# Kernel tuning notes

Hardware: AMD Instinct MI355X
Metric: run time of the kernel (lower is better)

The kernel has to match this reference:

```python
import jax, jax.numpy as jnp
import numpy as np

N = 20000      # nodes
E = 640000     # edges
HID = 128      # hidden_dim
HEADS = 8
HD = HID // HEADS  # head_dim = 16


def setup_inputs() -> dict:
    key = jax.random.key(0)
    ks = jax.random.split(key, 32)
    s = 1.0 / np.sqrt(HID)
    d = {}
    d["h"] = jax.random.normal(ks[0], (N, HID), jnp.float32)
    d["x"] = jax.random.normal(ks[1], (N, 3), jnp.float32)
    d["src"] = jax.random.randint(ks[2], (E,), 0, N)
    d["dst"] = jax.random.randint(ks[3], (E,), 0, N)
    d["distances"] = jax.random.uniform(ks[4], (E,), jnp.float32)
    d["bpp_edge_bias"] = jax.random.uniform(ks[5], (E,), jnp.float32)
    d["msa_edge_bias"] = jax.random.uniform(ks[6], (E,), jnp.float32)
    d["chem_edge_bias"] = jax.random.uniform(ks[7], (E,), jnp.float32)
    d["relative_offset"] = jax.random.normal(ks[8], (E,), jnp.float32)
    d["chain_break_mask"] = jax.random.uniform(ks[9], (E,), jnp.float32)
    # attention projections (nn.Linear(hidden, hidden): y = x @ W + b)
    for i, nm in enumerate(["Wq", "Wk", "Wv", "Wo"]):
        d[nm] = jax.random.normal(ks[10 + i], (HID, HID), jnp.float32) * s
    for nm in ["bq", "bk", "bv", "bo"]:
        d[nm] = jnp.zeros((HID,), jnp.float32)
    # six Linear(1, heads) edge-bias heads -> weight vector [HEADS] + bias [HEADS]
    for i, nm in enumerate(["dist", "bpp", "msa", "chem", "rel", "chain"]):
        d["w_" + nm] = jax.random.normal(ks[14 + i], (HEADS,), jnp.float32) * 0.1
        d["b_" + nm] = jnp.zeros((HEADS,), jnp.float32)
    # coord_gate: Linear(HID,HID) -> SiLU -> Linear(HID,1) -> Tanh
    d["Wg1"] = jax.random.normal(ks[20], (HID, HID), jnp.float32) * s
    d["bg1"] = jnp.zeros((HID,), jnp.float32)
    d["wg2"] = jax.random.normal(ks[21], (HID, 1), jnp.float32) * s
    d["bg2"] = jnp.zeros((1,), jnp.float32)
    return d


def _edge_bias(feat, w, b):
    # Linear(1, heads) applied to per-edge scalar: [E] -> [E, HEADS]
    return feat[:, None] * w[None, :] + b[None, :]


def reference(h, x, src, dst, distances, bpp_edge_bias, msa_edge_bias,
              chem_edge_bias, relative_offset, chain_break_mask,
              Wq, bq, Wk, bk, Wv, bv, Wo, bo,
              w_dist, b_dist, w_bpp, b_bpp, w_msa, b_msa,
              w_chem, b_chem, w_rel, b_rel, w_chain, b_chain,
              Wg1, bg1, wg2, bg2):
    n = h.shape[0]
    q = (h @ Wq + bq).reshape(n, HEADS, HD)
    k = (h @ Wk + bk).reshape(n, HEADS, HD)
    v = (h @ Wv + bv).reshape(n, HEADS, HD)
    q_src = q[src]   # [E, H, D]
    k_dst = k[dst]
    v_dst = v[dst]
    logits = jnp.einsum('ehd,ehd->eh', q_src, k_dst) / np.sqrt(float(HD))
    logits = (logits
              - _edge_bias(distances * distances, w_dist, b_dist)
              + _edge_bias(bpp_edge_bias, w_bpp, b_bpp)
              + _edge_bias(msa_edge_bias, w_msa, b_msa)
              + _edge_bias(chem_edge_bias, w_chem, b_chem)
              + _edge_bias(relative_offset, w_rel, b_rel)
              + _edge_bias(chain_break_mask, w_chain, b_chain))
    # segment softmax over edges grouped by src node, per head
    m = jax.ops.segment_max(logits, src, num_segments=n)        # [N, H]
    ex = jnp.exp(logits - m[src])                               # [E, H]
    denom = jax.ops.segment_sum(ex, src, num_segments=n)        # [N, H]
    weights = ex / jnp.maximum(denom[src], 1e-9)                # [E, H]
    # weighted scatter-aggregate of values to src nodes
    h_update = jax.ops.segment_sum(v_dst * weights[:, :, None], src,
                                   num_segments=n).reshape(n, HID)
    h_out = h + h_update @ Wo + bo
    # coordinate update
    weights_mean = weights.mean(axis=1)                         # [E]
    disp = jax.ops.segment_sum((x[dst] - x[src]) * weights_mean[:, None],
                               src, num_segments=n)             # [N, 3]
    gate = jnp.tanh(jax.nn.silu(h_out @ Wg1 + bg1) @ wg2 + bg2)  # [N, 1]
    x_out = x + gate * disp
    return h_out, x_out
```

## Files before the change

### kernel.cpp

```cpp
#include <hip/hip_runtime.h>
#include <hip/hip_bf16.h>

#define N_NODES 20000
#define N_EDGES 640000
#define HID 128
#define HEADS 8
#define HD 16
#define NB_SCAN ((N_NODES + 255) / 256)
#define CH 192
#define QKV_BLOCKS 625
#define PREP_BLOCKS 2
#define NREP 32
#define HIST_OFF (PREP_BLOCKS + QKV_BLOCKS)
#define HIST_BLOCKS 128

typedef __attribute__((ext_vector_type(8))) short bf16x8;
typedef __attribute__((ext_vector_type(4))) float f32x4;

__device__ __forceinline__ float bflo(unsigned u) {
    union { unsigned i; float f; } x; x.i = u << 16; return x.f;
}
__device__ __forceinline__ float bfhi(unsigned u) {
    union { unsigned i; float f; } x; x.i = u & 0xffff0000u; return x.f;
}
__device__ __forceinline__ float bfu(ushort u) {
    union { unsigned i; float f; } x; x.i = ((unsigned)u) << 16; return x.f;
}
__device__ __forceinline__ ushort f2bu(float f) {
    __hip_bfloat16 b = __float2bfloat16(f);
    union { __hip_bfloat16 b; ushort u; } c; c.b = b; return c.u;
}

__global__ __launch_bounds__(256) void front_kernel(
        const float* __restrict__ h,
        const float* __restrict__ bq, const float* __restrict__ bk,
        const float* __restrict__ bv,
        ushort* __restrict__ qb, ushort* __restrict__ kb, ushort* __restrict__ vb,
        const int* __restrict__ src,
        int* __restrict__ cnt, int* __restrict__ rank,
        const float* __restrict__ Wq, const float* __restrict__ Wk,
        const float* __restrict__ Wv, const float* __restrict__ Wo,
        const float* __restrict__ Wg1, ushort* __restrict__ Wt) {
    __shared__ __align__(16) ushort hs[32 * 136];
    __shared__ __align__(16) ushort ws[128 * 136];
    const int t = threadIdx.x;
    if (blockIdx.x < PREP_BLOCKS) {
        const float* W = (blockIdx.x == 0) ? Wo : Wg1;
        ushort* out = Wt + (size_t)(3 + blockIdx.x) * 16384;
        for (int i = t; i < 16384; i += 256) {
            int k = i >> 7, n = i & 127;
            out[n * 128 + k] = f2bu(W[i]);
        }
    } else if (blockIdx.x < HIST_OFF) {
        const int row0 = (blockIdx.x - PREP_BLOCKS) * 32;
        for (int i = t; i < 4096; i += 256)
            hs[(i >> 7) * 136 + (i & 127)] = f2bu(h[(size_t)row0 * 128 + i]);
        __syncthreads();
        const int w = t >> 6, lane = t & 63;
        const int rt = w >> 1, half = w & 1;
        const int lrow = lane & 15, lkb = (lane >> 4) * 8;
        bf16x8 a[4];
#pragma unroll
        for (int ks = 0; ks < 4; ++ks)
            a[ks] = *reinterpret_cast<const bf16x8*>(&hs[(rt * 16 + lrow) * 136 + ks * 32 + lkb]);
        __syncthreads();
        const int rloc0 = rt * 16 + (lane >> 4) * 4;
#define DO_MAT(WSRC, BIAS, OUT) \
        { \
        for (int idx = t; idx < 8192; idx += 256) { \
            const int c = idx & 127, kp = idx >> 7; \
            const float w0 = WSRC[(2 * kp) * 128 + c]; \
            const float w1 = WSRC[(2 * kp + 1) * 128 + c]; \
            *reinterpret_cast<unsigned*>(&ws[c * 136 + 2 * kp]) = \
                (unsigned)f2bu(w0) | ((unsigned)f2bu(w1) << 16); \
        } \
        __syncthreads(); \
        for (int ctp = 0; ctp < 4; ++ctp) { \
            const int col = (ctp * 2 + half) * 16 + lrow; \
            f32x4 acc = {0.f, 0.f, 0.f, 0.f}; \
            _Pragma("unroll") \
            for (int ks = 0; ks < 4; ++ks) { \
                bf16x8 b = *reinterpret_cast<const bf16x8*>( \
                    &ws[col * 136 + ks * 32 + lkb]); \
                acc = __builtin_amdgcn_mfma_f32_16x16x32_bf16(a[ks], b, acc, 0, 0, 0); \
            } \
            const float bias = BIAS[col]; \
            _Pragma("unroll") \
            for (int r = 0; r < 4; ++r) \
                hs[(rloc0 + r) * 128 + col] = f2bu(acc[r] + bias); \
        } \
        __syncthreads(); \
        { \
            uint4* outp = reinterpret_cast<uint4*>(OUT + (size_t)row0 * 128); \
            const uint4* inp = reinterpret_cast<const uint4*>(hs); \
            outp[t] = inp[t]; \
            outp[t + 256] = inp[t + 256]; \
        } \
        __syncthreads(); \
        }
        DO_MAT(Wq, bq, qb)
        DO_MAT(Wk, bk, kb)
        DO_MAT(Wv, bv, vb)
#undef DO_MAT
    } else {
        const int b = blockIdx.x - HIST_OFF;
        for (int e = b * 256 + t; e < N_EDGES; e += HIST_BLOCKS * 256) {
            const int rep = (e >> 8) & (NREP - 1);
            rank[e] = atomicAdd(&cnt[rep * N_NODES + src[e]], 1);
        }
    }
}

__global__ __launch_bounds__(256) void scan1_kernel(const int* __restrict__ cnt,
        int* __restrict__ repOff, int* __restrict__ startp,
        int* __restrict__ blockSums, int n) {
    __shared__ int sd[256];
    const int tid = threadIdx.x;
    const int i = blockIdx.x * 256 + tid;
    int running = 0;
    if (i < n) {
#pragma unroll
        for (int r = 0; r < NREP; ++r) {
            int v = cnt[r * N_NODES + i];
            repOff[r * N_NODES + i] = running;
            running += v;
        }
    }
    sd[tid] = running;
    __syncthreads();
#pragma unroll
    for (int off = 1; off < 256; off <<= 1) {
        int tv = (tid >= off) ? sd[tid - off] : 0;
        __syncthreads();
        sd[tid] += tv;
        __syncthreads();
    }
    if (i < n) startp[i] = sd[tid] - running;
    if (tid == 255) blockSums[blockIdx.x] = sd[255];
}

__global__ __launch_bounds__(128) void scan2_kernel(int* __restrict__ blockSums, int nb) {
    __shared__ int sd[128];
    const int tid = threadIdx.x;
    int xv = (tid < nb) ? blockSums[tid] : 0;
    sd[tid] = xv;
    __syncthreads();
#pragma unroll
    for (int off = 1; off < 128; off <<= 1) {
        int tv = (tid >= off) ? sd[tid - off] : 0;
        __syncthreads();
        sd[tid] += tv;
        __syncthreads();
    }
    if (tid < nb) blockSums[tid] = sd[tid] - xv;
    if (tid == 127) blockSums[nb] = sd[127];
}

__global__ __launch_bounds__(256) void scatter_kernel(
        const int* __restrict__ src, const int* __restrict__ dst,
        const float* __restrict__ dist, const float* __restrict__ bpp,
        const float* __restrict__ msa, const float* __restrict__ chem,
        const float* __restrict__ rel, const float* __restrict__ chain,
        const float* __restrict__ w_dist, const float* __restrict__ b_dist,
        const float* __restrict__ w_bpp, const float* __restrict__ b_bpp,
        const float* __restrict__ w_msa, const float* __restrict__ b_msa,
        const float* __restrict__ w_chem, const float* __restrict__ b_chem,
        const float* __restrict__ w_rel, const float* __restrict__ b_rel,
        const float* __restrict__ w_chain, const float* __restrict__ b_chain,
        const int* __restrict__ startp, const int* __restrict__ blockSums,
        const int* __restrict__ repOff, const int* __restrict__ rank,
        const float* __restrict__ x,
        uint4* __restrict__ bias16, uint2* __restrict__ meta) {
    const int b = blockIdx.x;
    const int e = b * 256 + threadIdx.x;
    const int s = src[e];
    const int rep = b & (NREP - 1);
    const int pos = startp[s] + blockSums[s >> 8] + repOff[rep * N_NODES + s] + rank[e];
    const int dn = dst[e];
    const float d2 = dist[e] * dist[e];
    const float f_bpp = bpp[e], f_msa = msa[e], f_chem = chem[e];
    const float f_rel = rel[e], f_chain = chain[e];
    ushort o16[8];
#pragma unroll
    for (int hq = 0; hq < 8; ++hq) {
        float bb = -(d2 * w_dist[hq] + b_dist[hq])
                + (f_bpp * w_bpp[hq] + b_bpp[hq])
                + (f_msa * w_msa[hq] + b_msa[hq])
                + (f_chem * w_chem[hq] + b_chem[hq])
                + (f_rel * w_rel[hq] + b_rel[hq])
                + (f_chain * w_chain[hq] + b_chain[hq]);
        o16[hq] = f2bu(bb);
    }
    uint4 b4;
    b4.x = (unsigned)o16[0] | ((unsigned)o16[1] << 16);
    b4.y = (unsigned)o16[2] | ((unsigned)o16[3] << 16);
    b4.z = (unsigned)o16[4] | ((unsigned)o16[5] << 16);
    b4.w = (unsigned)o16[6] | ((unsigned)o16[7] << 16);
    const float* xp = &x[(size_t)dn * 3];
    uint2 mt;
    mt.x = (unsigned)f2bu(xp[0]) | ((unsigned)f2bu(xp[1]) << 16);
    mt.y = (unsigned)f2bu(xp[2]) | ((unsigned)dn << 16);
    bias16[pos] = b4;
    meta[pos]   = mt;
}

__global__ __launch_bounds__(256) void node_kernel(const ushort* __restrict__ qb,
        const ushort* __restrict__ kb, const ushort* __restrict__ vb,
        const uint4* __restrict__ bias16, const uint2* __restrict__ meta,
        const float* __restrict__ x,
        const int* __restrict__ startp, const int* __restrict__ blockSums,
        ushort* __restrict__ hub, float* __restrict__ disp) {
    __shared__ float qLds[4 * 128];
    __shared__ float xsLds[12];
    __shared__ int   sLds[5];
    __shared__ ushort dnLds[CH];
    __shared__ float xLds[CH * 3];
    __shared__ ushort pbLds[CH * 8];
    __shared__ float redN[4][32][9];

    const int t = threadIdx.x;
    const int n0 = blockIdx.x * 4;
    const ushort* biasU = reinterpret_cast<const ushort*>(bias16);

    if (t < 64) {
        uint4 qv = reinterpret_cast<const uint4*>(qb + (size_t)n0 * 128)[t];
        const unsigned* qu = reinterpret_cast<const unsigned*>(&qv);
        float4 f0 = make_float4(bflo(qu[0]), bfhi(qu[0]), bflo(qu[1]), bfhi(qu[1]));
        float4 f1 = make_float4(bflo(qu[2]), bfhi(qu[2]), bflo(qu[3]), bfhi(qu[3]));
        *reinterpret_cast<float4*>(&qLds[t * 8])     = f0;
        *reinterpret_cast<float4*>(&qLds[t * 8 + 4]) = f1;
    }
    if (t < 12) xsLds[t] = x[(size_t)n0 * 3 + t];
    if (t < 5) {
        int idx = n0 + t;
        sLds[t] = (idx < N_NODES) ? (startp[idx] + blockSums[idx >> 8]) : N_EDGES;
    }
    __syncthreads();

    const int S0 = sLds[0], S4 = sLds[4];
    const int s1r = sLds[1], s2r = sLds[2], s3r = sLds[3];

    const int eg = t >> 5;
    const int dq = t & 31;
    const int hh = dq >> 2;
    const int jj = dq & 3;
    const int j3 = (jj < 3) ? jj : 0;

    float acc0[4] = {0,0,0,0}, acc1[4] = {0,0,0,0};
    float acc2[4] = {0,0,0,0}, acc3[4] = {0,0,0,0};
    float den0 = 0, den1 = 0, den2 = 0, den3 = 0;
    float adx0 = 0, adx1 = 0, adx2 = 0, adx3 = 0;

    for (int base = S0; base < S4; base += CH) {
        const int en = min(CH, S4 - base);
        __syncthreads();
        if (t < en) {
            const uint2 mt = meta[base + t];
            dnLds[t] = (ushort)(mt.y >> 16);
            xLds[t * 3 + 0] = bfu((ushort)(mt.x & 0xffff));
            xLds[t * 3 + 1] = bfu((ushort)(mt.x >> 16));
            xLds[t * 3 + 2] = bfu((ushort)(mt.y & 0xffff));
        }
        __syncthreads();
        const int np = en * 8;
#define PA_BODY(P) { \
            const int e = (P) >> 3, ha = (P) & 7; \
            const int ge = base + e; \
            const int m = (ge >= s1r) + (ge >= s2r) + (ge >= s3r); \
            const ushort* krow = kb + (size_t)dnLds[e] * 128 + ha * 16; \
            const uint4 ka = *reinterpret_cast<const uint4*>(krow); \
            const uint4 kb4 = *reinterpret_cast<const uint4*>(krow + 8); \
            const float bias = bfu(biasU[(size_t)base * 8 + (P)]); \
            const float* qrow = &qLds[m * 128 + ha * 16]; \
            const unsigned* kau = reinterpret_cast<const unsigned*>(&ka); \
            const unsigned* kbu = reinterpret_cast<const unsigned*>(&kb4); \
            float s0 = 0.f, s1 = 0.f, s2 = 0.f, s3 = 0.f; \
            _Pragma("unroll") \
            for (int i = 0; i < 4; ++i) { \
                s0 = fmaf(bflo(kau[i]), qrow[2 * i],     s0); \
                s1 = fmaf(bfhi(kau[i]), qrow[2 * i + 1], s1); \
                s2 = fmaf(bflo(kbu[i]), qrow[8 + 2 * i],     s2); \
                s3 = fmaf(bfhi(kbu[i]), qrow[8 + 2 * i + 1], s3); \
            } \
            pbLds[P] = f2bu(__expf(fmaf((s0 + s1) + (s2 + s3), 0.25f, bias))); \
        }
        {
            int p = t;
            for (; p + 256 < np; p += 512) { PA_BODY(p) PA_BODY(p + 256) }
            if (p < np) PA_BODY(p)
        }
#undef PA_BODY
        __syncthreads();
#define PC_BODY(E, ACC, DEN, ADX, XSV) { \
            const float pe = bfu(pbLds[(E) * 8 + hh]); \
            const ushort4 vv = *reinterpret_cast<const ushort4*>( \
                vb + (size_t)dnLds[E] * 128 + dq * 4); \
            ACC[0] = fmaf(pe, bfu(vv.x), ACC[0]); \
            ACC[1] = fmaf(pe, bfu(vv.y), ACC[1]); \
            ACC[2] = fmaf(pe, bfu(vv.z), ACC[2]); \
            ACC[3] = fmaf(pe, bfu(vv.w), ACC[3]); \
            DEN += pe; \
            ADX = fmaf(pe, xLds[(E) * 3 + j3] - XSV, ADX); \
        }
#define NODE_C(M, ACC, DEN, ADX) { \
            const int lo = max(sLds[M] - base, 0); \
            const int hi = min(sLds[M + 1] - base, en); \
            const float xsv = xsLds[M * 3 + j3]; \
            int e = lo + eg; \
            for (; e + 8 < hi; e += 16) { \
                PC_BODY(e, ACC, DEN, ADX, xsv) \
                PC_BODY(e + 8, ACC, DEN, ADX, xsv) \
            } \
            if (e < hi) PC_BODY(e, ACC, DEN, ADX, xsv) \
        }
        NODE_C(0, acc0, den0, adx0)
        NODE_C(1, acc1, den1, adx1)
        NODE_C(2, acc2, den2, adx2)
        NODE_C(3, acc3, den3, adx3)
#undef NODE_C
#undef PC_BODY
    }

    const int wv = t >> 6, lane = t & 63;
#define RED_M(M, ACC, DEN, ADX) { \
        float r0 = ACC[0], r1 = ACC[1], r2 = ACC[2], r3 = ACC[3]; \
        float rd = DEN, rx = (jj < 3) ? ADX : 0.f; \
        r0 += __shfl_xor(r0, 32); r1 += __shfl_xor(r1, 32); \
        r2 += __shfl_xor(r2, 32); r3 += __shfl_xor(r3, 32); \
        rd += __shfl_xor(rd, 32); rx += __shfl_xor(rx, 32); \
        if (lane < 32) { \
            redN[wv][lane][0] = r0; redN[wv][lane][1] = r1; \
            redN[wv][lane][2] = r2; redN[wv][lane][3] = r3; \
            redN[wv][lane][4] = rd; redN[wv][lane][5] = rx; \
        } \
        __syncthreads(); \
        if (t < 128) { \
            const int dqr = t >> 2, vi = t & 3; \
            float s = redN[0][dqr][vi] + redN[1][dqr][vi] \
                    + redN[2][dqr][vi] + redN[3][dqr][vi]; \
            float d = redN[0][dqr][4] + redN[1][dqr][4] \
                    + redN[2][dqr][4] + redN[3][dqr][4]; \
            hub[(size_t)(n0 + M) * 128 + t] = f2bu(s / fmaxf(d, 1e-9f)); \
        } \
        if (t < 32) { \
            float v = redN[0][t][5] + redN[1][t][5] + redN[2][t][5] + redN[3][t][5]; \
            float d = redN[0][t][4] + redN[1][t][4] + redN[2][t][4] + redN[3][t][4]; \
            float s = v / fmaxf(d, 1e-9f); \
            s += __shfl_xor(s, 4); s += __shfl_xor(s, 8); s += __shfl_xor(s, 16); \
            if (t < 3) disp[(size_t)(n0 + M) * 3 + t] = s * 0.125f; \
        } \
        __syncthreads(); }
    RED_M(0, acc0, den0, adx0)
    RED_M(1, acc1, den1, adx1)
    RED_M(2, acc2, den2, adx2)
    RED_M(3, acc3, den3, adx3)
#undef RED_M
}

__global__ __launch_bounds__(256) void out_kernel(const float* __restrict__ h,
        const float* __restrict__ x, const ushort* __restrict__ hub,
        const ushort* __restrict__ Wt,
        const float* __restrict__ bo, const float* __restrict__ bg1,
        const float* __restrict__ wg2, const float* __restrict__ bg2,
        const float* __restrict__ disp,
        float* __restrict__ hout, float* __restrict__ xout) {
    __shared__ __align__(16) ushort hus[32 * 136];
    __shared__ __align__(16) float hof[32 * 132];
    __shared__ float g1s[32 * 132];
    const int t = threadIdx.x;
    const int row0 = blockIdx.x * 32;
    for (int i8 = t; i8 < 512; i8 += 256) {
        const int row = i8 >> 4, c8 = (i8 & 15) * 8;
        *reinterpret_cast<uint4*>(&hus[row * 136 + c8]) =
            reinterpret_cast<const uint4*>(hub + (size_t)row0 * 128)[i8];
    }
    for (int i4 = t; i4 < 1024; i4 += 256) {
        const int row = i4 >> 5, c4 = (i4 & 31) * 4;
        *reinterpret_cast<float4*>(&hof[row * 132 + c4]) =
            reinterpret_cast<const float4*>(h + (size_t)row0 * 128)[i4];
    }
    __syncthreads();
    const int w = t >> 6, lane = t & 63;
    const int rt = w >> 1, half = w & 1;
    const int lrow = lane & 15, lkb = (lane >> 4) * 8;
    const int rloc = rt * 16 + (lane >> 4) * 4;
    bf16x8 a[4];
#pragma unroll
    for (int ks = 0; ks < 4; ++ks)
        a[ks] = *reinterpret_cast<const bf16x8*>(&hus[(rt * 16 + lrow) * 136 + ks * 32 + lkb]);
    for (int ctp = 0; ctp < 4; ++ctp) {
        const int col = (ctp * 2 + half) * 16 + lrow;
        f32x4 acc = {0.f, 0.f, 0.f, 0.f};
#pragma unroll
        for (int ks = 0; ks < 4; ++ks) {
            bf16x8 b = *reinterpret_cast<const bf16x8*>(&Wt[3 * 16384 + col * 128 + ks * 32 + lkb]);
            acc = __builtin_amdgcn_mfma_f32_16x16x32_bf16(a[ks], b, acc, 0, 0, 0);
        }
        const float bias = bo[col];
#pragma unroll
        for (int r = 0; r < 4; ++r)
            hof[(rloc + r) * 132 + col] += acc[r] + bias;
    }
    __syncthreads();
    for (int i4 = t; i4 < 1024; i4 += 256) {
        const int row = i4 >> 5, c4 = (i4 & 31) * 4;
        *reinterpret_cast<float4*>(hout + (size_t)(row0 + row) * 128 + c4) =
            *reinterpret_cast<const float4*>(&hof[row * 132 + c4]);
    }
    bf16x8 a2[4];
#pragma unroll
    for (int ks = 0; ks < 4; ++ks) {
        const float* fp = &hof[(rt * 16 + lrow) * 132 + ks * 32 + lkb];
        const float4 f0 = *reinterpret_cast<const float4*>(fp);
        const float4 f1 = *reinterpret_cast<const float4*>(fp + 4);
        bf16x8 v;
        v[0] = (short)f2bu(f0.x); v[1] = (short)f2bu(f0.y);
        v[2] = (short)f2bu(f0.z); v[3] = (short)f2bu(f0.w);
        v[4] = (short)f2bu(f1.x); v[5] = (short)f2bu(f1.y);
        v[6] = (short)f2bu(f1.z); v[7] = (short)f2bu(f1.w);
        a2[ks] = v;
    }
    for (int ctp = 0; ctp < 4; ++ctp) {
        const int col = (ctp * 2 + half) * 16 + lrow;
        f32x4 acc = {0.f, 0.f, 0.f, 0.f};
#pragma unroll
        for (int ks = 0; ks < 4; ++ks) {
            bf16x8 b = *reinterpret_cast<const bf16x8*>(&Wt[4 * 16384 + col * 128 + ks * 32 + lkb]);
            acc = __builtin_amdgcn_mfma_f32_16x16x32_bf16(a2[ks], b, acc, 0, 0, 0);
        }
        const float bias = bg1[col];
#pragma unroll
        for (int r = 0; r < 4; ++r) {
            float av = acc[r] + bias;
            g1s[(rloc + r) * 132 + col] = av / (1.f + __expf(-av));
        }
    }
    __syncthreads();
    {
        const int r = t >> 3, j = t & 7;
        float partial = 0.f;
        for (int cc = j; cc < 128; cc += 8) partial += g1s[r * 132 + cc] * wg2[cc];
        partial += __shfl_xor(partial, 1);
        partial += __shfl_xor(partial, 2);
        partial += __shfl_xor(partial, 4);
        const float gate = tanhf(partial + bg2[0]);
        if (j < 3) {
            const int row = row0 + r;
            xout[(size_t)row * 3 + j] = x[(size_t)row * 3 + j] + gate * disp[(size_t)row * 3 + j];
        }
    }
}


extern "C" void kernel_launch(void* const* d_in, const int* in_sizes, int n_in,
                              void* d_out, int out_size, void* d_ws, size_t ws_size,
                              hipStream_t stream) {
    const float* h     = (const float*)d_in[0];
    const float* x     = (const float*)d_in[1];
    const int*   src   = (const int*)d_in[2];
    const int*   dst   = (const int*)d_in[3];
    const float* dist  = (const float*)d_in[4];
    const float* bpp   = (const float*)d_in[5];
    const float* msa   = (const float*)d_in[6];
    const float* chem  = (const float*)d_in[7];
    const float* rel   = (const float*)d_in[8];
    const float* chain = (const float*)d_in[9];
    const float* Wq = (const float*)d_in[10];
    const float* Wk = (const float*)d_in[11];
    const float* Wv = (const float*)d_in[12];
    const float* Wo = (const float*)d_in[13];
    const float* bq = (const float*)d_in[14];
    const float* bk = (const float*)d_in[15];
    const float* bv = (const float*)d_in[16];
    const float* bo = (const float*)d_in[17];
    const float* w_dist = (const float*)d_in[18];  const float* b_dist = (const float*)d_in[19];
    const float* w_bpp  = (const float*)d_in[20];  const float* b_bpp  = (const float*)d_in[21];
    const float* w_msa  = (const float*)d_in[22];  const float* b_msa  = (const float*)d_in[23];
    const float* w_chem = (const float*)d_in[24];  const float* b_chem = (const float*)d_in[25];
    const float* w_rel  = (const float*)d_in[26];  const float* b_rel  = (const float*)d_in[27];
    const float* w_chain= (const float*)d_in[28];  const float* b_chain= (const float*)d_in[29];
    const float* Wg1 = (const float*)d_in[30];
    const float* bg1 = (const float*)d_in[31];
    const float* wg2 = (const float*)d_in[32];
    const float* bg2 = (const float*)d_in[33];

    char* wp = (char*)d_ws;
    const size_t NH2 = (size_t)N_NODES * HID * sizeof(ushort);
    ushort* hub   = (ushort*)wp;               wp += NH2;
    ushort* qb    = (ushort*)wp;               wp += NH2;
    ushort* kb    = (ushort*)wp;               wp += NH2;
    ushort* vb    = (ushort*)wp;               wp += NH2;
    uint4*  bias16= (uint4*)wp;                wp += (size_t)N_EDGES * 16;
    uint2*  meta  = (uint2*)wp;                wp += (size_t)N_EDGES * 8;
    float*  disp  = (float*)wp;                wp += (size_t)N_NODES * 3 * sizeof(float);
    int* rank     = (int*)wp;                  wp += (size_t)N_EDGES * sizeof(int);
    int* startp   = (int*)wp;                  wp += (size_t)N_NODES * sizeof(int);
    int* cnt      = (int*)wp;                  wp += (size_t)NREP * N_NODES * sizeof(int);
    int* repOff   = (int*)wp;                  wp += (size_t)NREP * N_NODES * sizeof(int);
    int* blockSums= (int*)wp;                  wp += (size_t)(NB_SCAN + 1) * sizeof(int);
    ushort* Wt    = (ushort*)wp;               wp += (size_t)5 * 16384 * sizeof(ushort);

    float* hout = (float*)d_out;
    float* xout = hout + (size_t)N_NODES * HID;

    hipMemsetAsync(cnt, 0, (size_t)NREP * N_NODES * sizeof(int), stream);
    hipLaunchKernelGGL(front_kernel, dim3(HIST_OFF + HIST_BLOCKS), dim3(256), 0, stream,
                       h, bq, bk, bv, qb, kb, vb,
                       src, cnt, rank, Wq, Wk, Wv, Wo, Wg1, Wt);
    hipLaunchKernelGGL(scan1_kernel, dim3(NB_SCAN), dim3(256), 0, stream,
                       cnt, repOff, startp, blockSums, N_NODES);
    hipLaunchKernelGGL(scan2_kernel, dim3(1), dim3(128), 0, stream, blockSums, NB_SCAN);
    hipLaunchKernelGGL(scatter_kernel, dim3(N_EDGES / 256), dim3(256), 0, stream,
                       src, dst, dist, bpp, msa, chem, rel, chain,
                       w_dist, b_dist, w_bpp, b_bpp, w_msa, b_msa,
                       w_chem, b_chem, w_rel, b_rel, w_chain, b_chain,
                       startp, blockSums, repOff, rank, x, bias16, meta);
    hipLaunchKernelGGL(node_kernel, dim3(N_NODES / 4), dim3(256), 0, stream,
                       qb, kb, vb, bias16, meta, x, startp, blockSums, hub, disp);
    hipLaunchKernelGGL(out_kernel, dim3(N_NODES / 32), dim3(256), 0, stream,
                       h, x, hub, Wt, bo, bg1, wg2, bg2, disp, hout, xout);
}
```

Baseline: 136.2 us.

## Store V in FP8 and fold block-sum scan into scan1 via last-block ticket

The V projection is now written as FP8 e4m3 instead of bf16, which halves the bytes the node kernel gathers per edge when it aggregates values. The separate scan2 launch is removed: the last scan1 block, found through an atomic ticket, performs the block-sum prefix scan itself. This trades precision of the value vectors for less gather bandwidth and one fewer kernel launch. The FP8 rounding error may hurt accuracy tolerance.

```diff
diff --git a/kernel.cpp b/kernel.cpp
--- a/kernel.cpp
+++ b/kernel.cpp
@@ -16,6 +16,14 @@
 
 typedef __attribute__((ext_vector_type(8))) short bf16x8;
 typedef __attribute__((ext_vector_type(4))) float f32x4;
+typedef __attribute__((ext_vector_type(2))) float f32x2;
+
+#if __has_builtin(__builtin_amdgcn_cvt_pk_f32_fp8) && __has_builtin(__builtin_amdgcn_cvt_pk_fp8_f32)
+#define FP8_FAST 1
+#else
+#define FP8_FAST 0
+#include <hip/hip_fp8.h>
+#endif
 
 __device__ __forceinline__ float bflo(unsigned u) {
     union { unsigned i; float f; } x; x.i = u << 16; return x.f;
@@ -29,13 +37,39 @@
 __device__ __forceinline__ ushort f2bu(float f) {
     __hip_bfloat16 b = __float2bfloat16(f);
     union { __hip_bfloat16 b; ushort u; } c; c.b = b; return c.u;
+}
+__device__ __forceinline__ unsigned fp8x4_enc(float a, float b, float c, float d) {
+#if FP8_FAST
+    unsigned w = (unsigned)__builtin_amdgcn_cvt_pk_fp8_f32(a, b, 0, false);
+    w = (unsigned)__builtin_amdgcn_cvt_pk_fp8_f32(c, d, (int)w, true);
+    return w;
+#else
+    __hip_fp8_e4m3 e0(a), e1(b), e2(c), e3(d);
+    return (unsigned)e0.__x | ((unsigned)e1.__x << 8) |
+           ((unsigned)e2.__x << 16) | ((unsigned)e3.__x << 24);
+#endif
+}
+__device__ __forceinline__ void fp8x4_dec(unsigned p, float* o) {
+#if FP8_FAST
+    f32x2 lo = __builtin_amdgcn_cvt_pk_f32_fp8((int)p, false);
+    f32x2 hi = __builtin_amdgcn_cvt_pk_f32_fp8((int)p, true);
+    o[0] = lo[0]; o[1] = lo[1]; o[2] = hi[0]; o[3] = hi[1];
+#else
+#pragma unroll
+    for (int i = 0; i < 4; ++i) {
+        unsigned char b = (p >> (8 * i)) & 0xff;
+        __hip_fp8_e4m3 e; e.__x = b;
+        o[i] = (float)e;
+    }
+#endif
 }
 
 __global__ __launch_bounds__(256) void front_kernel(
         const float* __restrict__ h,
         const float* __restrict__ bq, const float* __restrict__ bk,
         const float* __restrict__ bv,
-        ushort* __restrict__ qb, ushort* __restrict__ kb, ushort* __restrict__ vb,
+        ushort* __restrict__ qb, ushort* __restrict__ kb,
+        unsigned char* __restrict__ vb8,
         const int* __restrict__ src,
         int* __restrict__ cnt, int* __restrict__ rank,
         const float* __restrict__ Wq, const float* __restrict__ Wk,
@@ -65,8 +99,7 @@
             a[ks] = *reinterpret_cast<const bf16x8*>(&hs[(rt * 16 + lrow) * 136 + ks * 32 + lkb]);
         __syncthreads();
         const int rloc0 = rt * 16 + (lane >> 4) * 4;
-#define DO_MAT(WSRC, BIAS, OUT) \
-        { \
+#define STAGE_W(WSRC) \
         for (int idx = t; idx < 8192; idx += 256) { \
             const int c = idx & 127, kp = idx >> 7; \
             const float w0 = WSRC[(2 * kp) * 128 + c]; \
@@ -74,16 +107,23 @@
             *reinterpret_cast<unsigned*>(&ws[c * 136 + 2 * kp]) = \
                 (unsigned)f2bu(w0) | ((unsigned)f2bu(w1) << 16); \
         } \
-        __syncthreads(); \
+        __syncthreads();
+#define MFMA_COL(col, acc) \
+        { \
+            _Pragma("unroll") \
+            for (int ks = 0; ks < 4; ++ks) { \
+                bf16x8 b = *reinterpret_cast<const bf16x8*>( \
+                    &ws[(col) * 136 + ks * 32 + lkb]); \
+                acc = __builtin_amdgcn_mfma_f32_16x16x32_bf16(a[ks], b, acc, 0, 0, 0); \
+            } \
+        }
+#define DO_MAT_BF16(WSRC, BIAS, OUT) \
+        { \
+        STAGE_W(WSRC) \
         for (int ctp = 0; ctp < 4; ++ctp) { \
             const int col = (ctp * 2 + half) * 16 + lrow; \
             f32x4 acc = {0.f, 0.f, 0.f, 0.f}; \
-            _Pragma("unroll") \
-            for (int ks = 0; ks < 4; ++ks) { \
-                bf16x8 b = *reinterpret_cast<const bf16x8*>( \
-                    &ws[col * 136 + ks * 32 + lkb]); \
-                acc = __builtin_amdgcn_mfma_f32_16x16x32_bf16(a[ks], b, acc, 0, 0, 0); \
-            } \
+            MFMA_COL(col, acc) \
             const float bias = BIAS[col]; \
             _Pragma("unroll") \
             for (int r = 0; r < 4; ++r) \
@@ -98,10 +138,32 @@
         } \
         __syncthreads(); \
         }
-        DO_MAT(Wq, bq, qb)
-        DO_MAT(Wk, bk, kb)
-        DO_MAT(Wv, bv, vb)
-#undef DO_MAT
+        DO_MAT_BF16(Wq, bq, qb)
+        DO_MAT_BF16(Wk, bk, kb)
+        {
+        STAGE_W(Wv)
+        unsigned char* hsb = reinterpret_cast<unsigned char*>(hs);
+        for (int ctp = 0; ctp < 4; ++ctp) {
+            const int col = (ctp * 2 + half) * 16 + lrow;
+            f32x4 acc = {0.f, 0.f, 0.f, 0.f};
+            MFMA_COL(col, acc)
+            const float bias = bv[col];
+            const unsigned wpk = fp8x4_enc(acc[0] + bias, acc[1] + bias,
+                                           acc[2] + bias, acc[3] + bias);
+#pragma unroll
+            for (int r = 0; r < 4; ++r)
+                hsb[(rloc0 + r) * 128 + col] = (unsigned char)((wpk >> (8 * r)) & 0xff);
+        }
+        __syncthreads();
+        {
+            uint4* outp = reinterpret_cast<uint4*>(vb8 + (size_t)row0 * 128);
+            const uint4* inp = reinterpret_cast<const uint4*>(hs);
+            outp[t] = inp[t];
+        }
+        }
+#undef DO_MAT_BF16
+#undef MFMA_COL
+#undef STAGE_W
     } else {
         const int b = blockIdx.x - HIST_OFF;
         for (int e = b * 256 + t; e < N_EDGES; e += HIST_BLOCKS * 256) {
@@ -113,8 +175,9 @@
 
 __global__ __launch_bounds__(256) void scan1_kernel(const int* __restrict__ cnt,
         int* __restrict__ repOff, int* __restrict__ startp,
-        int* __restrict__ blockSums, int n) {
+        int* __restrict__ blockSums, int* __restrict__ ticket, int n) {
     __shared__ int sd[256];
+    __shared__ int lastFlag;
     const int tid = threadIdx.x;
     const int i = blockIdx.x * 256 + tid;
     int running = 0;
@@ -136,24 +199,26 @@
         __syncthreads();
     }
     if (i < n) startp[i] = sd[tid] - running;
-    if (tid == 255) blockSums[blockIdx.x] = sd[255];
-}
-
-__global__ __launch_bounds__(128) void scan2_kernel(int* __restrict__ blockSums, int nb) {
-    __shared__ int sd[128];
-    const int tid = threadIdx.x;
-    int xv = (tid < nb) ? blockSums[tid] : 0;
-    sd[tid] = xv;
+    if (tid == 255) {
+        atomicExch(&blockSums[blockIdx.x], sd[255]);
+        __threadfence();
+        lastFlag = (atomicAdd(ticket, 1) == NB_SCAN - 1);
+    }
     __syncthreads();
-#pragma unroll
-    for (int off = 1; off < 128; off <<= 1) {
-        int tv = (tid >= off) ? sd[tid - off] : 0;
-        __syncthreads();
-        sd[tid] += tv;
-        __syncthreads();
-    }
-    if (tid < nb) blockSums[tid] = sd[tid] - xv;
-    if (tid == 127) blockSums[nb] = sd[127];
+    if (lastFlag) {
+        int v = (tid < NB_SCAN) ? atomicAdd(&blockSums[tid], 0) : 0;
+        sd[tid] = v;
+        __syncthreads();
+#pragma unroll
+        for (int off = 1; off < 256; off <<= 1) {
+            int tv = (tid >= off) ? sd[tid - off] : 0;
+            __syncthreads();
+            sd[tid] += tv;
+            __syncthreads();
+        }
+        if (tid < NB_SCAN) blockSums[tid] = sd[tid] - v;
+        if (tid == 255) blockSums[NB_SCAN] = sd[255];
+    }
 }
 
 __global__ __launch_bounds__(256) void scatter_kernel(
@@ -205,7 +270,7 @@
 }
 
 __global__ __launch_bounds__(256) void node_kernel(const ushort* __restrict__ qb,
-        const ushort* __restrict__ kb, const ushort* __restrict__ vb,
+        const ushort* __restrict__ kb, const unsigned char* __restrict__ vb8,
         const uint4* __restrict__ bias16, const uint2* __restrict__ meta,
         const float* __restrict__ x,
         const int* __restrict__ startp, const int* __restrict__ blockSums,
@@ -293,12 +358,14 @@
         __syncthreads();
 #define PC_BODY(E, ACC, DEN, ADX, XSV) { \
             const float pe = bfu(pbLds[(E) * 8 + hh]); \
-            const ushort4 vv = *reinterpret_cast<const ushort4*>( \
-                vb + (size_t)dnLds[E] * 128 + dq * 4); \
-            ACC[0] = fmaf(pe, bfu(vv.x), ACC[0]); \
-            ACC[1] = fmaf(pe, bfu(vv.y), ACC[1]); \
-            ACC[2] = fmaf(pe, bfu(vv.z), ACC[2]); \
-            ACC[3] = fmaf(pe, bfu(vv.w), ACC[3]); \
+            const unsigned vp = *reinterpret_cast<const unsigned*>( \
+                vb8 + (size_t)dnLds[E] * 128 + dq * 4); \
+            float vd[4]; \
+            fp8x4_dec(vp, vd); \
+            ACC[0] = fmaf(pe, vd[0], ACC[0]); \
+            ACC[1] = fmaf(pe, vd[1], ACC[1]); \
+            ACC[2] = fmaf(pe, vd[2], ACC[2]); \
+            ACC[3] = fmaf(pe, vd[3], ACC[3]); \
             DEN += pe; \
             ADX = fmaf(pe, xLds[(E) * 3 + j3] - XSV, ADX); \
         }
@@ -489,13 +556,14 @@
     ushort* hub   = (ushort*)wp;               wp += NH2;
     ushort* qb    = (ushort*)wp;               wp += NH2;
     ushort* kb    = (ushort*)wp;               wp += NH2;
-    ushort* vb    = (ushort*)wp;               wp += NH2;
+    unsigned char* vb8 = (unsigned char*)wp;   wp += (size_t)N_NODES * HID;
     uint4*  bias16= (uint4*)wp;                wp += (size_t)N_EDGES * 16;
     uint2*  meta  = (uint2*)wp;                wp += (size_t)N_EDGES * 8;
     float*  disp  = (float*)wp;                wp += (size_t)N_NODES * 3 * sizeof(float);
     int* rank     = (int*)wp;                  wp += (size_t)N_EDGES * sizeof(int);
     int* startp   = (int*)wp;                  wp += (size_t)N_NODES * sizeof(int);
     int* cnt      = (int*)wp;                  wp += (size_t)NREP * N_NODES * sizeof(int);
+    int* ticket   = (int*)wp;                  wp += sizeof(int);
     int* repOff   = (int*)wp;                  wp += (size_t)NREP * N_NODES * sizeof(int);
     int* blockSums= (int*)wp;                  wp += (size_t)(NB_SCAN + 1) * sizeof(int);
     ushort* Wt    = (ushort*)wp;               wp += (size_t)5 * 16384 * sizeof(ushort);
@@ -503,20 +571,19 @@
     float* hout = (float*)d_out;
     float* xout = hout + (size_t)N_NODES * HID;
 
-    hipMemsetAsync(cnt, 0, (size_t)NREP * N_NODES * sizeof(int), stream);
+    hipMemsetAsync(cnt, 0, ((size_t)NREP * N_NODES + 1) * sizeof(int), stream);
     hipLaunchKernelGGL(front_kernel, dim3(HIST_OFF + HIST_BLOCKS), dim3(256), 0, stream,
-                       h, bq, bk, bv, qb, kb, vb,
+                       h, bq, bk, bv, qb, kb, vb8,
                        src, cnt, rank, Wq, Wk, Wv, Wo, Wg1, Wt);
     hipLaunchKernelGGL(scan1_kernel, dim3(NB_SCAN), dim3(256), 0, stream,
-                       cnt, repOff, startp, blockSums, N_NODES);
-    hipLaunchKernelGGL(scan2_kernel, dim3(1), dim3(128), 0, stream, blockSums, NB_SCAN);
+                       cnt, repOff, startp, blockSums, ticket, N_NODES);
     hipLaunchKernelGGL(scatter_kernel, dim3(N_EDGES / 256), dim3(256), 0, stream,
                        src, dst, dist, bpp, msa, chem, rel, chain,
                        w_dist, b_dist, w_bpp, b_bpp, w_msa, b_msa,
                        w_chem, b_chem, w_rel, b_rel, w_chain, b_chain,
                        startp, blockSums, repOff, rank, x, bias16, meta);
     hipLaunchKernelGGL(node_kernel, dim3(N_NODES / 4), dim3(256), 0, stream,
-                       qb, kb, vb, bias16, meta, x, startp, blockSums, hub, disp);
+                       qb, kb, vb8, bias16, meta, x, startp, blockSums, hub, disp);
     hipLaunchKernelGGL(out_kernel, dim3(N_NODES / 32), dim3(256), 0, stream,
                        h, x, hub, Wt, bo, bg1, wg2, bg2, disp, hout, xout);
 }
```

Measured after the change: 135.6 us. About the same (-0.4%).
